# Performance work log

Measured on AMD Instinct MI355X. Metric: run time of the kernel, lower is better.

## Reference

```python
import jax, jax.numpy as jnp
import numpy as np

N_NODES = 100000


def gcn_layer(x, W, b, src, dst, n):
    # PyG GCNConv: h = x @ W, then D^{-1/2}(A+I)D^{-1/2} aggregation, then + b
    h = x @ W  # [N, out]
    ones = jnp.ones(src.shape[0], dtype=h.dtype)
    deg = jax.ops.segment_sum(ones, dst, num_segments=n) + 1.0  # +1 for self loop
    dinv = jax.lax.rsqrt(deg)  # [N]
    norm = dinv[src] * dinv[dst]  # [E]
    msgs = h[src] * norm[:, None]  # gather + scale, [E, out]
    agg = jax.ops.segment_sum(msgs, dst, num_segments=n)
    agg = agg + h * (dinv * dinv)[:, None]  # self-loop term
    return agg + b


def setup_inputs() -> dict:
    key = jax.random.key(0)
    k1, k2, k3, k4, k5, k6 = jax.random.split(key, 6)
    in_dim, h1, h2 = 256, 128, 64
    x = jax.random.normal(k1, (N_NODES, in_dim), dtype=jnp.float32)
    edge_index = jax.random.randint(k2, (2, 1600000), 0, N_NODES, dtype=jnp.int64)
    # Glorot-style init for weights, zeros for bias (PyG default)
    W1 = jax.random.normal(k3, (in_dim, h1), dtype=jnp.float32) / np.sqrt(in_dim)
    b1 = jnp.zeros((h1,), dtype=jnp.float32)
    W2 = jax.random.normal(k4, (h1, h2), dtype=jnp.float32) / np.sqrt(h1)
    b2 = jnp.zeros((h2,), dtype=jnp.float32)
    return {"x": x, "W1": W1, "b1": b1, "W2": W2, "b2": b2, "edge_index": edge_index}


def reference(x, W1, b1, W2, b2, edge_index):
    src, dst = edge_index[0], edge_index[1]
    n = x.shape[0]
    h = jax.nn.relu(gcn_layer(x, W1, b1, src, dst, n))
    h = jax.nn.relu(gcn_layer(h, W2, b2, src, dst, n))
    return h
```

## Files before the change

### kernel.cpp

```cpp
#include <hip/hip_runtime.h>
#include <hip/hip_bf16.h>


typedef __attribute__((ext_vector_type(8))) short bf16x8;
typedef __attribute__((ext_vector_type(4))) float f32x4;

__device__ inline unsigned short f2bf(float f) {
    unsigned u = __float_as_uint(f);
    u = (u + 0x7fff + ((u >> 16) & 1)) >> 16;
    return (unsigned short)u;
}
__device__ inline float bf2f(unsigned short h) {
    return __uint_as_float(((unsigned)h) << 16);
}
__device__ inline float bflo(unsigned u) { return __uint_as_float(u << 16); }
__device__ inline float bfhi(unsigned u) { return __uint_as_float(u & 0xffff0000u); }

__global__ void hist_kernel(const int* __restrict__ dst, int* __restrict__ deg, int E) {
    int stride = gridDim.x * blockDim.x;
    for (int i = blockIdx.x * blockDim.x + threadIdx.x; i < E; i += stride)
        atomicAdd(&deg[dst[i]], 1);
}

__global__ __launch_bounds__(1024) void scan_partial_kernel(const int* __restrict__ deg,
        int* __restrict__ psum, float* __restrict__ dinv, int n) {
    __shared__ int wsum[16];
    int tid = threadIdx.x, wave = tid >> 6, lane = tid & 63;
    int i0 = blockIdx.x * 4096 + tid * 4;
    int v0 = 0, v1 = 0, v2 = 0, v3 = 0;
    if (i0 + 3 < n) {
        int4 v = *(const int4*)(deg + i0);
        v0 = v.x; v1 = v.y; v2 = v.z; v3 = v.w;
    } else {
        if (i0 + 0 < n) v0 = deg[i0 + 0];
        if (i0 + 1 < n) v1 = deg[i0 + 1];
        if (i0 + 2 < n) v2 = deg[i0 + 2];
        if (i0 + 3 < n) v3 = deg[i0 + 3];
    }
    if (i0 + 0 < n) dinv[i0 + 0] = 1.0f / sqrtf((float)v0 + 1.0f);
    if (i0 + 1 < n) dinv[i0 + 1] = 1.0f / sqrtf((float)v1 + 1.0f);
    if (i0 + 2 < n) dinv[i0 + 2] = 1.0f / sqrtf((float)v2 + 1.0f);
    if (i0 + 3 < n) dinv[i0 + 3] = 1.0f / sqrtf((float)v3 + 1.0f);
    int s = v0 + v1 + v2 + v3;
    #pragma unroll
    for (int off = 1; off < 64; off <<= 1) s += __shfl_xor(s, off, 64);
    if (lane == 0) wsum[wave] = s;
    __syncthreads();
    if (tid == 0) {
        int t = 0;
        #pragma unroll
        for (int w = 0; w < 16; ++w) t += wsum[w];
        psum[blockIdx.x] = t;
    }
}

__global__ void scan_base_kernel(int* __restrict__ psum, int* __restrict__ offs,
                                 int nb, int n) {
    int lane = threadIdx.x;
    int v = (lane < nb) ? psum[lane] : 0;
    int x = v;
    #pragma unroll
    for (int off = 1; off < 64; off <<= 1) {
        int y = __shfl_up(x, off, 64);
        if (lane >= off) x += y;
    }
    if (lane < nb) psum[lane] = x - v;
    if (lane == 63) offs[n] = x;
}

__global__ __launch_bounds__(1024) void scan_local_kernel(const int* __restrict__ deg,
        const int* __restrict__ psum, int* __restrict__ offs, int n) {
    __shared__ int wsum[16];
    int tid = threadIdx.x, wave = tid >> 6, lane = tid & 63;
    int i0 = blockIdx.x * 4096 + tid * 4;
    int v0 = 0, v1 = 0, v2 = 0, v3 = 0;
    if (i0 + 3 < n) {
        int4 v = *(const int4*)(deg + i0);
        v0 = v.x; v1 = v.y; v2 = v.z; v3 = v.w;
    } else {
        if (i0 + 0 < n) v0 = deg[i0 + 0];
        if (i0 + 1 < n) v1 = deg[i0 + 1];
        if (i0 + 2 < n) v2 = deg[i0 + 2];
        if (i0 + 3 < n) v3 = deg[i0 + 3];
    }
    int s = v0 + v1 + v2 + v3;
    int x = s;
    #pragma unroll
    for (int off = 1; off < 64; off <<= 1) {
        int y = __shfl_up(x, off, 64);
        if (lane >= off) x += y;
    }
    if (lane == 63) wsum[wave] = x;
    __syncthreads();
    int wbase = 0;
    #pragma unroll
    for (int w = 0; w < 16; ++w)
        if (w < wave) wbase += wsum[w];
    int ex = psum[blockIdx.x] + wbase + (x - s);
    if (i0 + 0 < n) offs[i0 + 0] = ex;
    if (i0 + 1 < n) offs[i0 + 1] = ex + v0;
    if (i0 + 2 < n) offs[i0 + 2] = ex + v0 + v1;
    if (i0 + 3 < n) offs[i0 + 3] = ex + v0 + v1 + v2;
}

__global__ void fill_kernel(const int* __restrict__ src, const int* __restrict__ dst,
        const int* __restrict__ offs, int* __restrict__ cursor,
        int* __restrict__ csr, int E) {
    int stride = gridDim.x * blockDim.x;
    for (int i = blockIdx.x * blockDim.x + threadIdx.x; i < E; i += stride) {
        int d = dst[i];
        int pos = offs[d] + atomicAdd(&cursor[d], 1);
        csr[pos] = src[i];
    }
}

__global__ void wsplit_kernel(const float* __restrict__ W,
        unsigned short* __restrict__ Wt_hi, unsigned short* __restrict__ Wt_lo,
        int K, int N) {
    int idx = blockIdx.x * 256 + threadIdx.x;
    if (idx >= K * N) return;
    int k = idx / N, n = idx - k * N;
    float v = W[idx];
    unsigned short h = f2bf(v);
    unsigned short l = f2bf(v - bf2f(h));
    Wt_hi[(size_t)n * K + k] = h;
    Wt_lo[(size_t)n * K + k] = l;
}

template <int K, int NT>
__global__ __launch_bounds__(256) void gemm_mfma_kernel(const float* __restrict__ X,
        const unsigned short* __restrict__ Wt_hi, const unsigned short* __restrict__ Wt_lo,
        const float* __restrict__ dinv, unsigned short* __restrict__ G, int M) {
    constexpr int N   = NT * 16;
    constexpr int BK  = 32;
    constexpr int LDA = BK + 8;
    __shared__ unsigned short Ah[128 * LDA];
    __shared__ unsigned short Al[128 * LDA];

    const int tid  = threadIdx.x;
    const int wv   = tid >> 6, ln = tid & 63;
    const int l16  = ln & 15, kseg = ln >> 4;
    const int brow = blockIdx.x * 128;

    f32x4 acc[2][NT];
    #pragma unroll
    for (int a = 0; a < 2; ++a)
        #pragma unroll
        for (int b = 0; b < NT; ++b) acc[a][b] = 0;

    const int srow = tid >> 1;
    const int scol = (tid & 1) * 16;
    int grow = brow + srow;
    if (grow >= M) grow = M - 1;
    const float* xrow = X + (size_t)grow * K + scol;
    unsigned int* ahw = (unsigned int*)&Ah[srow * LDA + scol];
    unsigned int* alw = (unsigned int*)&Al[srow * LDA + scol];

    const int arow = wv * 32;

    for (int k0 = 0; k0 < K; k0 += BK) {
        float4 q0 = *(const float4*)(xrow + k0 + 0);
        float4 q1 = *(const float4*)(xrow + k0 + 4);
        float4 q2 = *(const float4*)(xrow + k0 + 8);
        float4 q3 = *(const float4*)(xrow + k0 + 12);
        float v[16] = {q0.x,q0.y,q0.z,q0.w, q1.x,q1.y,q1.z,q1.w,
                       q2.x,q2.y,q2.z,q2.w, q3.x,q3.y,q3.z,q3.w};
        unsigned hw[8], lw[8];
        #pragma unroll
        for (int j = 0; j < 8; ++j) {
            unsigned short h0 = f2bf(v[2*j]),   h1 = f2bf(v[2*j+1]);
            unsigned short l0 = f2bf(v[2*j]   - bf2f(h0));
            unsigned short l1 = f2bf(v[2*j+1] - bf2f(h1));
            hw[j] = (unsigned)h0 | ((unsigned)h1 << 16);
            lw[j] = (unsigned)l0 | ((unsigned)l1 << 16);
        }
        *(uint4*)(ahw + 0) = make_uint4(hw[0], hw[1], hw[2], hw[3]);
        *(uint4*)(ahw + 4) = make_uint4(hw[4], hw[5], hw[6], hw[7]);
        *(uint4*)(alw + 0) = make_uint4(lw[0], lw[1], lw[2], lw[3]);
        *(uint4*)(alw + 4) = make_uint4(lw[4], lw[5], lw[6], lw[7]);
        __syncthreads();

        bf16x8 a_h[2], a_l[2];
        #pragma unroll
        for (int tr = 0; tr < 2; ++tr) {
            a_h[tr] = *(const bf16x8*)&Ah[(arow + tr * 16 + l16) * LDA + kseg * 8];
            a_l[tr] = *(const bf16x8*)&Al[(arow + tr * 16 + l16) * LDA + kseg * 8];
        }
        #pragma unroll
        for (int tc = 0; tc < NT; ++tc) {
            size_t wo = (size_t)(tc * 16 + l16) * K + k0 + kseg * 8;
            bf16x8 b_h = *(const bf16x8*)(Wt_hi + wo);
            bf16x8 b_l = *(const bf16x8*)(Wt_lo + wo);
            #pragma unroll
            for (int tr = 0; tr < 2; ++tr) {
                acc[tr][tc] = __builtin_amdgcn_mfma_f32_16x16x32_bf16(a_h[tr], b_h, acc[tr][tc], 0, 0, 0);
                acc[tr][tc] = __builtin_amdgcn_mfma_f32_16x16x32_bf16(a_l[tr], b_h, acc[tr][tc], 0, 0, 0);
                acc[tr][tc] = __builtin_amdgcn_mfma_f32_16x16x32_bf16(a_h[tr], b_l, acc[tr][tc], 0, 0, 0);
            }
        }
        __syncthreads();
    }

    #pragma unroll
    for (int tr = 0; tr < 2; ++tr) {
        int rbase = brow + arow + tr * 16 + (ln >> 4) * 4;
        #pragma unroll
        for (int r = 0; r < 4; ++r) {
            int row = rbase + r;
            if (row < M) {
                float dv = dinv[row];
                #pragma unroll
                for (int tc = 0; tc < NT; ++tc)
                    G[(size_t)row * N + tc * 16 + l16] = f2bf(acc[tr][tc][r] * dv);
            }
        }
    }
}

__global__ __launch_bounds__(256) void aggregate128_kernel(const unsigned* __restrict__ G,
        const int* __restrict__ csr, const int* __restrict__ offs,
        const float* __restrict__ dinv, const float* __restrict__ bias,
        float* __restrict__ out, int n) {
    int wave = threadIdx.x >> 6, lane = threadIdx.x & 63;
    int node = blockIdx.x * 4 + wave;
    if (node >= n) return;
    int beg = offs[node], end = offs[node + 1];

    unsigned u = G[(size_t)node * 64 + lane];
    float a0 = bflo(u), a1 = bfhi(u);
    int e = beg;
    for (; e + 4 <= end; e += 4) {
        int s0 = csr[e], s1 = csr[e + 1], s2 = csr[e + 2], s3 = csr[e + 3];
        unsigned u0 = G[(size_t)s0 * 64 + lane];
        unsigned u1 = G[(size_t)s1 * 64 + lane];
        unsigned u2 = G[(size_t)s2 * 64 + lane];
        unsigned u3 = G[(size_t)s3 * 64 + lane];
        a0 += (bflo(u0) + bflo(u1)) + (bflo(u2) + bflo(u3));
        a1 += (bfhi(u0) + bfhi(u1)) + (bfhi(u2) + bfhi(u3));
    }
    for (; e < end; ++e) {
        unsigned u0 = G[(size_t)csr[e] * 64 + lane];
        a0 += bflo(u0);
        a1 += bfhi(u0);
    }
    float di = dinv[node];
    float2 r;
    r.x = fmaxf(fmaf(a0, di, bias[lane * 2 + 0]), 0.0f);
    r.y = fmaxf(fmaf(a1, di, bias[lane * 2 + 1]), 0.0f);
    ((float2*)(out + (size_t)node * 128))[lane] = r;
}

__global__ __launch_bounds__(256) void aggregate64_kernel(const unsigned* __restrict__ G,
        const int* __restrict__ csr, const int* __restrict__ offs,
        const float* __restrict__ dinv, const float* __restrict__ bias,
        float* __restrict__ out, int n) {
    int wave = threadIdx.x >> 6, lane = threadIdx.x & 63;
    int node = blockIdx.x * 4 + wave;
    if (node >= n) return;
    int beg = offs[node], end = offs[node + 1];
    int half = lane >> 5, col = lane & 31;

    float a0 = 0.0f, a1 = 0.0f;
    if (half == 0) {
        unsigned u = G[(size_t)node * 32 + col];
        a0 = bflo(u); a1 = bfhi(u);
    }
    int e = beg;
    for (; e + 4 <= end; e += 4) {
        int sA = csr[e + half], sB = csr[e + 2 + half];
        unsigned uA = G[(size_t)sA * 32 + col];
        unsigned uB = G[(size_t)sB * 32 + col];
        a0 += bflo(uA) + bflo(uB);
        a1 += bfhi(uA) + bfhi(uB);
    }
    if (e + 2 <= end) {
        int sA = csr[e + half];
        unsigned uA = G[(size_t)sA * 32 + col];
        a0 += bflo(uA);
        a1 += bfhi(uA);
        e += 2;
    }
    if (e < end && half == 0) {
        unsigned uA = G[(size_t)csr[e] * 32 + col];
        a0 += bflo(uA);
        a1 += bfhi(uA);
    }
    a0 += __shfl_down(a0, 32, 64);
    a1 += __shfl_down(a1, 32, 64);
    if (half == 0) {
        float di = dinv[node];
        float2 r;
        r.x = fmaxf(fmaf(a0, di, bias[col * 2 + 0]), 0.0f);
        r.y = fmaxf(fmaf(a1, di, bias[col * 2 + 1]), 0.0f);
        ((float2*)(out + (size_t)node * 64))[col] = r;
    }
}

extern "C" void kernel_launch(void* const* d_in, const int* in_sizes, int n_in,
                              void* d_out, int out_size, void* d_ws, size_t ws_size,
                              hipStream_t stream) {
    const float* x  = (const float*)d_in[0];
    const float* W1 = (const float*)d_in[1];
    const float* b1 = (const float*)d_in[2];
    const float* W2 = (const float*)d_in[3];
    const float* b2 = (const float*)d_in[4];
    const int* edge = (const int*)d_in[5];

    const int IN = 256, H1 = 128, H2 = 64;
    const int E = in_sizes[5] / 2;
    const int N = in_sizes[0] / IN;
    const int* srcp = edge;
    const int* dstp = edge + E;

    char* ws = (char*)d_ws;
    auto alignup = [](size_t v) { return (v + 255) & ~(size_t)255; };
    size_t off = 0;
    size_t degSz = alignup((size_t)N * 4);
    int*            deg    = (int*)(ws + off);            off += degSz;
    int*            cursor = (int*)(ws + off);            off += degSz;
    int*            offs   = (int*)(ws + off);            off += alignup(((size_t)N + 1) * 4);
    float*          dinv   = (float*)(ws + off);          off += degSz;
    int*            psum   = (int*)(ws + off);            off += alignup(64 * 4);
    int*            csr    = (int*)(ws + off);            off += alignup((size_t)E * 4);
    unsigned short* wt1h   = (unsigned short*)(ws + off); off += alignup((size_t)IN * H1 * 2);
    unsigned short* wt1l   = (unsigned short*)(ws + off); off += alignup((size_t)IN * H1 * 2);
    unsigned short* wt2h   = (unsigned short*)(ws + off); off += alignup((size_t)H1 * H2 * 2);
    unsigned short* wt2l   = (unsigned short*)(ws + off); off += alignup((size_t)H1 * H2 * 2);
    unsigned short* g1     = (unsigned short*)(ws + off); off += alignup((size_t)N * H1 * 2);
    float*          h1     = (float*)(ws + off);          off += alignup((size_t)N * H1 * 4);
    unsigned short* g2     = g1;

    hipMemsetAsync(deg, 0, 2 * degSz, stream);

    int egrid = (E + 255) / 256;
    if (egrid > 2048) egrid = 2048;
    int sb = (N + 4095) / 4096;

    hist_kernel<<<egrid, 256, 0, stream>>>(dstp, deg, E);
    scan_partial_kernel<<<sb, 1024, 0, stream>>>(deg, psum, dinv, N);
    scan_base_kernel<<<1, 64, 0, stream>>>(psum, offs, sb, N);
    scan_local_kernel<<<sb, 1024, 0, stream>>>(deg, psum, offs, N);
    fill_kernel<<<egrid, 256, 0, stream>>>(srcp, dstp, offs, cursor, csr, E);
    wsplit_kernel<<<(IN * H1 + 255) / 256, 256, 0, stream>>>(W1, wt1h, wt1l, IN, H1);
    wsplit_kernel<<<(H1 * H2 + 255) / 256, 256, 0, stream>>>(W2, wt2h, wt2l, H1, H2);

    int mgrid = (N + 127) / 128;
    int agrid = (N + 3) / 4;

    gemm_mfma_kernel<256, 8><<<mgrid, 256, 0, stream>>>(x, wt1h, wt1l, dinv, g1, N);
    aggregate128_kernel<<<agrid, 256, 0, stream>>>((const unsigned*)g1, csr, offs,
                                                   dinv, b1, h1, N);
    gemm_mfma_kernel<128, 4><<<mgrid, 256, 0, stream>>>(h1, wt2h, wt2l, dinv, g2, N);
    aggregate64_kernel<<<agrid, 256, 0, stream>>>((const unsigned*)g2, csr, offs,
                                                  dinv, b2, (float*)d_out, N);
}
```

Baseline: 558.9 us.

## Fuse prep and fill/GEMM1 kernels, store layer-1 output as bf16, drop LDS staging

```diff
diff --git a/kernel.cpp b/kernel.cpp
--- a/kernel.cpp
+++ b/kernel.cpp
@@ -15,11 +15,46 @@
 }
 __device__ inline float bflo(unsigned u) { return __uint_as_float(u << 16); }
 __device__ inline float bfhi(unsigned u) { return __uint_as_float(u & 0xffff0000u); }
-
-__global__ void hist_kernel(const int* __restrict__ dst, int* __restrict__ deg, int E) {
-    int stride = gridDim.x * blockDim.x;
-    for (int i = blockIdx.x * blockDim.x + threadIdx.x; i < E; i += stride)
-        atomicAdd(&deg[dst[i]], 1);
+__device__ inline unsigned pack_bf16_2(float lo, float hi) {
+    return (unsigned)f2bf(lo) | ((unsigned)f2bf(hi) << 16);
+}
+__device__ inline void cvt8(const float* v, bf16x8& h8, bf16x8& l8) {
+    #pragma unroll
+    for (int j = 0; j < 8; ++j) {
+        unsigned short h = f2bf(v[j]);
+        h8[j] = (short)h;
+        l8[j] = (short)f2bf(v[j] - bf2f(h));
+    }
+}
+
+__global__ void prep_kernel(const int* __restrict__ dst, int* __restrict__ deg, int E,
+        const float* __restrict__ W1, unsigned short* __restrict__ w1h,
+        unsigned short* __restrict__ w1l,
+        const float* __restrict__ W2, unsigned short* __restrict__ w2h,
+        unsigned short* __restrict__ w2l) {
+    const int W1B = (256 * 128) / 256;
+    const int W2B = (128 * 64) / 256;
+    int b = blockIdx.x;
+    if (b < W1B) {
+        int idx = b * 256 + threadIdx.x;
+        int k = idx >> 7, n = idx & 127;
+        float v = W1[idx];
+        unsigned short h = f2bf(v);
+        w1h[(size_t)n * 256 + k] = h;
+        w1l[(size_t)n * 256 + k] = f2bf(v - bf2f(h));
+    } else if (b < W1B + W2B) {
+        int idx = (b - W1B) * 256 + threadIdx.x;
+        int k = idx >> 6, n = idx & 63;
+        float v = W2[idx];
+        unsigned short h = f2bf(v);
+        w2h[(size_t)n * 128 + k] = h;
+        w2l[(size_t)n * 128 + k] = f2bf(v - bf2f(h));
+    } else {
+        int nb = gridDim.x - (W1B + W2B);
+        int stride = nb * 256;
+        for (int i = (b - W1B - W2B) * 256 + threadIdx.x; i < E; i += stride)
+            atomicAdd(&deg[dst[i]], 1);
+    }
 }
 
 __global__ __launch_bounds__(1024) void scan_partial_kernel(const int* __restrict__ deg,
@@ -103,115 +138,132 @@
     if (i0 + 3 < n) offs[i0 + 3] = ex + v0 + v1 + v2;
 }
 
-__global__ void fill_kernel(const int* __restrict__ src, const int* __restrict__ dst,
+__global__ __launch_bounds__(256) void fused_fill_gemm1(
+        const int* __restrict__ src, const int* __restrict__ dst,
         const int* __restrict__ offs, int* __restrict__ cursor,
-        int* __restrict__ csr, int E) {
-    int stride = gridDim.x * blockDim.x;
-    for (int i = blockIdx.x * blockDim.x + threadIdx.x; i < E; i += stride) {
-        int d = dst[i];
-        int pos = offs[d] + atomicAdd(&cursor[d], 1);
-        csr[pos] = src[i];
-    }
-}
-
-__global__ void wsplit_kernel(const float* __restrict__ W,
-        unsigned short* __restrict__ Wt_hi, unsigned short* __restrict__ Wt_lo,
-        int K, int N) {
-    int idx = blockIdx.x * 256 + threadIdx.x;
-    if (idx >= K * N) return;
-    int k = idx / N, n = idx - k * N;
-    float v = W[idx];
-    unsigned short h = f2bf(v);
-    unsigned short l = f2bf(v - bf2f(h));
-    Wt_hi[(size_t)n * K + k] = h;
-    Wt_lo[(size_t)n * K + k] = l;
-}
-
-template <int K, int NT>
-__global__ __launch_bounds__(256) void gemm_mfma_kernel(const float* __restrict__ X,
-        const unsigned short* __restrict__ Wt_hi, const unsigned short* __restrict__ Wt_lo,
+        int* __restrict__ csr, int E, int NF,
+        const float* __restrict__ X,
+        const unsigned short* __restrict__ Wh, const unsigned short* __restrict__ Wl,
         const float* __restrict__ dinv, unsigned short* __restrict__ G, int M) {
-    constexpr int N   = NT * 16;
-    constexpr int BK  = 32;
-    constexpr int LDA = BK + 8;
-    __shared__ unsigned short Ah[128 * LDA];
-    __shared__ unsigned short Al[128 * LDA];
-
-    const int tid  = threadIdx.x;
-    const int wv   = tid >> 6, ln = tid & 63;
-    const int l16  = ln & 15, kseg = ln >> 4;
-    const int brow = blockIdx.x * 128;
-
-    f32x4 acc[2][NT];
+    if ((int)blockIdx.x < NF) {
+        int stride = NF * 256;
+        for (int i = blockIdx.x * 256 + threadIdx.x; i < E; i += stride) {
+            int d = dst[i];
+            int pos = offs[d] + atomicAdd(&cursor[d], 1);
+            csr[pos] = src[i];
+        }
+        return;
+    }
+    constexpr int K = 256;
+    const int bid = blockIdx.x - NF;
+    const int tid = threadIdx.x;
+    const int wv = tid >> 6, ln = tid & 63;
+    const int l16 = ln & 15, kseg = ln >> 4;
+    const int r0 = bid * 128 + wv * 32;
+
+    int rA0 = r0 + l16;       if (rA0 >= M) rA0 = M - 1;
+    int rA1 = r0 + 16 + l16;  if (rA1 >= M) rA1 = M - 1;
+    const float* pA0 = X + (size_t)rA0 * K + kseg * 8;
+    const float* pA1 = X + (size_t)rA1 * K + kseg * 8;
+
+    f32x4 acc[2][8];
     #pragma unroll
     for (int a = 0; a < 2; ++a)
         #pragma unroll
-        for (int b = 0; b < NT; ++b) acc[a][b] = 0;
-
-    const int srow = tid >> 1;
-    const int scol = (tid & 1) * 16;
-    int grow = brow + srow;
-    if (grow >= M) grow = M - 1;
-    const float* xrow = X + (size_t)grow * K + scol;
-    unsigned int* ahw = (unsigned int*)&Ah[srow * LDA + scol];
-    unsigned int* alw = (unsigned int*)&Al[srow * LDA + scol];
-
-    const int arow = wv * 32;
-
-    for (int k0 = 0; k0 < K; k0 += BK) {
-        float4 q0 = *(const float4*)(xrow + k0 + 0);
-        float4 q1 = *(const float4*)(xrow + k0 + 4);
-        float4 q2 = *(const float4*)(xrow + k0 + 8);
-        float4 q3 = *(const float4*)(xrow + k0 + 12);
-        float v[16] = {q0.x,q0.y,q0.z,q0.w, q1.x,q1.y,q1.z,q1.w,
-                       q2.x,q2.y,q2.z,q2.w, q3.x,q3.y,q3.z,q3.w};
-        unsigned hw[8], lw[8];
-        #pragma unroll
-        for (int j = 0; j < 8; ++j) {
-            unsigned short h0 = f2bf(v[2*j]),   h1 = f2bf(v[2*j+1]);
-            unsigned short l0 = f2bf(v[2*j]   - bf2f(h0));
-            unsigned short l1 = f2bf(v[2*j+1] - bf2f(h1));
-            hw[j] = (unsigned)h0 | ((unsigned)h1 << 16);
-            lw[j] = (unsigned)l0 | ((unsigned)l1 << 16);
-        }
-        *(uint4*)(ahw + 0) = make_uint4(hw[0], hw[1], hw[2], hw[3]);
-        *(uint4*)(ahw + 4) = make_uint4(hw[4], hw[5], hw[6], hw[7]);
-        *(uint4*)(alw + 0) = make_uint4(lw[0], lw[1], lw[2], lw[3]);
-        *(uint4*)(alw + 4) = make_uint4(lw[4], lw[5], lw[6], lw[7]);
-        __syncthreads();
-
-        bf16x8 a_h[2], a_l[2];
-        #pragma unroll
-        for (int tr = 0; tr < 2; ++tr) {
-            a_h[tr] = *(const bf16x8*)&Ah[(arow + tr * 16 + l16) * LDA + kseg * 8];
-            a_l[tr] = *(const bf16x8*)&Al[(arow + tr * 16 + l16) * LDA + kseg * 8];
-        }
-        #pragma unroll
-        for (int tc = 0; tc < NT; ++tc) {
+        for (int b = 0; b < 8; ++b) acc[a][b] = 0;
+
+    #pragma unroll 2
+    for (int k0 = 0; k0 < K; k0 += 32) {
+        bf16x8 ah[2], al[2];
+        {
+            float4 qa = *(const float4*)(pA0 + k0);
+            float4 qb = *(const float4*)(pA0 + k0 + 4);
+            float v[8] = {qa.x, qa.y, qa.z, qa.w, qb.x, qb.y, qb.z, qb.w};
+            cvt8(v, ah[0], al[0]);
+        }
+        {
+            float4 qa = *(const float4*)(pA1 + k0);
+            float4 qb = *(const float4*)(pA1 + k0 + 4);
+            float v[8] = {qa.x, qa.y, qa.z, qa.w, qb.x, qb.y, qb.z, qb.w};
+            cvt8(v, ah[1], al[1]);
+        }
+        #pragma unroll
+        for (int tc = 0; tc < 8; ++tc) {
             size_t wo = (size_t)(tc * 16 + l16) * K + k0 + kseg * 8;
-            bf16x8 b_h = *(const bf16x8*)(Wt_hi + wo);
-            bf16x8 b_l = *(const bf16x8*)(Wt_lo + wo);
+            bf16x8 bh = *(const bf16x8*)(Wh + wo);
+            bf16x8 bl = *(const bf16x8*)(Wl + wo);
             #pragma unroll
             for (int tr = 0; tr < 2; ++tr) {
-                acc[tr][tc] = __builtin_amdgcn_mfma_f32_16x16x32_bf16(a_h[tr], b_h, acc[tr][tc], 0, 0, 0);
-                acc[tr][tc] = __builtin_amdgcn_mfma_f32_16x16x32_bf16(a_l[tr], b_h, acc[tr][tc], 0, 0, 0);
-                acc[tr][tc] = __builtin_amdgcn_mfma_f32_16x16x32_bf16(a_h[tr], b_l, acc[tr][tc], 0, 0, 0);
+                acc[tr][tc] = __builtin_amdgcn_mfma_f32_16x16x32_bf16(ah[tr], bh, acc[tr][tc], 0, 0, 0);
+                acc[tr][tc] = __builtin_amdgcn_mfma_f32_16x16x32_bf16(al[tr], bh, acc[tr][tc], 0, 0, 0);
+                acc[tr][tc] = __builtin_amdgcn_mfma_f32_16x16x32_bf16(ah[tr], bl, acc[tr][tc], 0, 0, 0);
             }
         }
-        __syncthreads();
     }
 
     #pragma unroll
     for (int tr = 0; tr < 2; ++tr) {
-        int rbase = brow + arow + tr * 16 + (ln >> 4) * 4;
+        int rbase = r0 + tr * 16 + (ln >> 4) * 4;
         #pragma unroll
         for (int r = 0; r < 4; ++r) {
             int row = rbase + r;
             if (row < M) {
                 float dv = dinv[row];
                 #pragma unroll
-                for (int tc = 0; tc < NT; ++tc)
-                    G[(size_t)row * N + tc * 16 + l16] = f2bf(acc[tr][tc][r] * dv);
+                for (int tc = 0; tc < 8; ++tc)
+                    G[(size_t)row * 128 + tc * 16 + l16] = f2bf(acc[tr][tc][r] * dv);
+            }
+        }
+    }
+}
+
+__global__ __launch_bounds__(256) void gemm2_kernel(const unsigned short* __restrict__ H,
+        const unsigned short* __restrict__ Wh, const unsigned short* __restrict__ Wl,
+        const float* __restrict__ dinv, unsigned short* __restrict__ G, int M) {
+    constexpr int K = 128;
+    const int tid = threadIdx.x;
+    const int wv = tid >> 6, ln = tid & 63;
+    const int l16 = ln & 15, kseg = ln >> 4;
+    const int r0 = blockIdx.x * 128 + wv * 32;
+
+    int rA0 = r0 + l16;       if (rA0 >= M) rA0 = M - 1;
+    int rA1 = r0 + 16 + l16;  if (rA1 >= M) rA1 = M - 1;
+    const unsigned short* pA0 = H + (size_t)rA0 * K + kseg * 8;
+    const unsigned short* pA1 = H + (size_t)rA1 * K + kseg * 8;
+
+    f32x4 acc[2][4];
+    #pragma unroll
+    for (int a = 0; a < 2; ++a)
+        #pragma unroll
+        for (int b = 0; b < 4; ++b) acc[a][b] = 0;
+
+    #pragma unroll
+    for (int k0 = 0; k0 < K; k0 += 32) {
+        bf16x8 a0 = *(const bf16x8*)(pA0 + k0);
+        bf16x8 a1 = *(const bf16x8*)(pA1 + k0);
+        #pragma unroll
+        for (int tc = 0; tc < 4; ++tc) {
+            size_t wo = (size_t)(tc * 16 + l16) * K + k0 + kseg * 8;
+            bf16x8 bh = *(const bf16x8*)(Wh + wo);
+            bf16x8 bl = *(const bf16x8*)(Wl + wo);
+            acc[0][tc] = __builtin_amdgcn_mfma_f32_16x16x32_bf16(a0, bh, acc[0][tc], 0, 0, 0);
+            acc[0][tc] = __builtin_amdgcn_mfma_f32_16x16x32_bf16(a0, bl, acc[0][tc], 0, 0, 0);
+            acc[1][tc] = __builtin_amdgcn_mfma_f32_16x16x32_bf16(a1, bh, acc[1][tc], 0, 0, 0);
+            acc[1][tc] = __builtin_amdgcn_mfma_f32_16x16x32_bf16(a1, bl, acc[1][tc], 0, 0, 0);
+        }
+    }
+
+    #pragma unroll
+    for (int tr = 0; tr < 2; ++tr) {
+        int rbase = r0 + tr * 16 + (ln >> 4) * 4;
+        #pragma unroll
+        for (int r = 0; r < 4; ++r) {
+            int row = rbase + r;
+            if (row < M) {
+                float dv = dinv[row];
+                #pragma unroll
+                for (int tc = 0; tc < 4; ++tc)
+                    G[(size_t)row * 64 + tc * 16 + l16] = f2bf(acc[tr][tc][r] * dv);
             }
         }
     }
@@ -220,7 +272,7 @@
 __global__ __launch_bounds__(256) void aggregate128_kernel(const unsigned* __restrict__ G,
         const int* __restrict__ csr, const int* __restrict__ offs,
         const float* __restrict__ dinv, const float* __restrict__ bias,
-        float* __restrict__ out, int n) {
+        unsigned* __restrict__ out, int n) {
     int wave = threadIdx.x >> 6, lane = threadIdx.x & 63;
     int node = blockIdx.x * 4 + wave;
     if (node >= n) return;
@@ -244,10 +296,9 @@
         a1 += bfhi(u0);
     }
     float di = dinv[node];
-    float2 r;
-    r.x = fmaxf(fmaf(a0, di, bias[lane * 2 + 0]), 0.0f);
-    r.y = fmaxf(fmaf(a1, di, bias[lane * 2 + 1]), 0.0f);
-    ((float2*)(out + (size_t)node * 128))[lane] = r;
+    float rx = fmaxf(fmaf(a0, di, bias[lane * 2 + 0]), 0.0f);
+    float ry = fmaxf(fmaf(a1, di, bias[lane * 2 + 1]), 0.0f);
+    out[(size_t)node * 64 + lane] = pack_bf16_2(rx, ry);
 }
 
 __global__ __launch_bounds__(256) void aggregate64_kernel(const unsigned* __restrict__ G,
@@ -327,30 +378,30 @@
     unsigned short* wt2h   = (unsigned short*)(ws + off); off += alignup((size_t)H1 * H2 * 2);
     unsigned short* wt2l   = (unsigned short*)(ws + off); off += alignup((size_t)H1 * H2 * 2);
     unsigned short* g1     = (unsigned short*)(ws + off); off += alignup((size_t)N * H1 * 2);
-    float*          h1     = (float*)(ws + off);          off += alignup((size_t)N * H1 * 4);
+    unsigned*       h1b    = (unsigned*)(ws + off);       off += alignup((size_t)N * (H1 / 2) * 4);
     unsigned short* g2     = g1;
 
     hipMemsetAsync(deg, 0, 2 * degSz, stream);
 
-    int egrid = (E + 255) / 256;
-    if (egrid > 2048) egrid = 2048;
+    int hgrid = 2048;
     int sb = (N + 4095) / 4096;
 
-    hist_kernel<<<egrid, 256, 0, stream>>>(dstp, deg, E);
+    prep_kernel<<<160 + hgrid, 256, 0, stream>>>(dstp, deg, E, W1, wt1h, wt1l,
+                                                 W2, wt2h, wt2l);
     scan_partial_kernel<<<sb, 1024, 0, stream>>>(deg, psum, dinv, N);
     scan_base_kernel<<<1, 64, 0, stream>>>(psum, offs, sb, N);
     scan_local_kernel<<<sb, 1024, 0, stream>>>(deg, psum, offs, N);
-    fill_kernel<<<egrid, 256, 0, stream>>>(srcp, dstp, offs, cursor, csr, E);
-    wsplit_kernel<<<(IN * H1 + 255) / 256, 256, 0, stream>>>(W1, wt1h, wt1l, IN, H1);
-    wsplit_kernel<<<(H1 * H2 + 255) / 256, 256, 0, stream>>>(W2, wt2h, wt2l, H1, H2);
-
-    int mgrid = (N + 127) / 128;
+
+    const int NF = 1024;
+    const int NG = (N + 127) / 128;
+    fused_fill_gemm1<<<NF + NG, 256, 0, stream>>>(srcp, dstp, offs, cursor, csr, E,
+                                                  NF, x, wt1h, wt1l, dinv, g1, N);
+
     int agrid = (N + 3) / 4;
-
-    gemm_mfma_kernel<256, 8><<<mgrid, 256, 0, stream>>>(x, wt1h, wt1l, dinv, g1, N);
     aggregate128_kernel<<<agrid, 256, 0, stream>>>((const unsigned*)g1, csr, offs,
-                                                   dinv, b1, h1, N);
-    gemm_mfma_kernel<128, 4><<<mgrid, 256, 0, stream>>>(h1, wt2h, wt2l, dinv, g2, N);
+                                                   dinv, b1, h1b, N);
+    gemm2_kernel<<<NG, 256, 0, stream>>>((const unsigned short*)h1b, wt2h, wt2l,
+                                         dinv, g2, N);
     aggregate64_kernel<<<agrid, 256, 0, stream>>>((const unsigned*)g2, csr, offs,
                                                   dinv, b2, (float*)d_out, N);
 }
```

New measurement: 526.1 us. 5.9% less time.
